# Optimization experiments

Measured on AMD Instinct MI355X. Metric: run time of the kernel, lower is better.

The kernel has to match this reference:

```python
import jax, jax.numpy as jnp
import numpy as np

ATT_RAW = 312
HID = 900
ATT_DIM = 4096


def setup_inputs() -> dict:
    key = jax.random.key(0)
    ks = jax.random.split(key, 12)
    B, S, N, C = 4, 128, 50, ATT_DIM
    x = jax.random.normal(ks[0], (B, S, C), dtype=jnp.float32)
    x_label = jax.random.randint(ks[1], (B, S), 0, N, dtype=jnp.int64)
    att = jax.random.normal(ks[2], (B, N, ATT_RAW), dtype=jnp.float32)
    att_label = jax.random.randint(ks[3], (B, N), 0, N, dtype=jnp.int64)
    def lin(k, out_f, in_f):
        bound = 1.0 / np.sqrt(in_f)
        kw, kb = jax.random.split(k)
        W = jax.random.uniform(kw, (out_f, in_f), jnp.float32, -bound, bound)
        b = jax.random.uniform(kb, (out_f,), jnp.float32, -bound, bound)
        return W, b
    W1, b1 = lin(ks[4], HID, ATT_RAW)       # attnet layer 1
    W2, b2 = lin(ks[5], ATT_DIM, HID)       # attnet layer 2
    W3, b3 = lin(ks[6], HID, 2 * ATT_DIM)   # o layer 1
    W4, b4 = lin(ks[7], 1, HID)             # o layer 2
    return {"x": x, "x_label": x_label, "att": att, "att_label": att_label,
            "W1": W1, "b1": b1, "W2": W2, "b2": b2,
            "W3": W3, "b3": b3, "W4": W4, "b4": b4}


def reference(x, x_label, att, att_label, W1, b1, W2, b2, W3, b3, W4, b4):
    # x: [B,S,C], att: [B,N,312]; train=True branch -> scalar MSE loss
    B, S, C = x.shape
    N = att.shape[1]
    # attnet: 312 -> 900 -> 4096 with ReLU
    att_f = jax.nn.relu(jax.nn.relu(att @ W1.T + b1) @ W2.T + b2)  # [B,N,4096]
    # o layer 1 on concat([x_f, att_f]) == split matmul + broadcast add
    W3x, W3a = W3[:, :C], W3[:, C:]
    hx = jnp.einsum('bsc,hc->bsh', x, W3x)        # [B,S,900]
    ha = jnp.einsum('bnc,hc->bnh', att_f, W3a)    # [B,N,900]
    pre = jax.nn.relu(hx[:, :, None, :] + ha[:, None, :, :] + b3)  # [B,S,N,900]
    score = jax.nn.sigmoid(jnp.einsum('bsnh,h->bsn', pre, W4[0]) + b4[0])  # [B,S,N]
    label = (x_label[:, :, None] == att_label[:, None, :]).astype(score.dtype)
    loss = jnp.sum((label - score) ** 2) / B / S
    return loss
```

## Files before the change

### kernel.cpp

```cpp
#include <hip/hip_runtime.h>
#include <hip/hip_bf16.h>

typedef __attribute__((ext_vector_type(8))) short bf16x8;
typedef __attribute__((ext_vector_type(4))) float f32x4;
typedef __attribute__((ext_vector_type(8))) unsigned short u16x8;

__device__ __forceinline__ void gload16(const void* g, void* l) {
    __builtin_amdgcn_global_load_lds((const __attribute__((address_space(1))) void*)g,
                                     (__attribute__((address_space(3))) void*)l, 16, 0, 0);
}
__device__ __forceinline__ float bf2f(unsigned short u) {
    union { unsigned i; float f; } v; v.i = ((unsigned)u) << 16; return v.f;
}
__device__ __forceinline__ unsigned short f2bf(float f) {
    __hip_bfloat16 h = __float2bfloat16(f);
    return *(unsigned short*)&h;
}

template<int ROWS>
__device__ __forceinline__ void stage_f32(
    const float* __restrict__ src, int ld, int row0, int rmax,
    int k0, int kmax, short* __restrict__ lds, int tid)
{
    #pragma unroll
    for (int i = 0; i < ROWS / 32; ++i) {
        const int ch = i * 256 + tid;
        const int r = ch >> 3;
        const int kc8 = (ch & 7) * 8;
        const int gr = row0 + r;
        const int gk = k0 + kc8;
        u16x8 v;
        if (gr < rmax && gk + 8 <= kmax) {
            const float* s = src + (size_t)gr * ld + gk;
            const float4 f0 = *(const float4*)s;
            const float4 f1 = *(const float4*)(s + 4);
            const float ff[8] = {f0.x, f0.y, f0.z, f0.w, f1.x, f1.y, f1.z, f1.w};
            #pragma unroll
            for (int j = 0; j < 8; ++j) v[j] = f2bf(ff[j]);
        } else if (gr < rmax && gk < kmax) {
            #pragma unroll
            for (int j = 0; j < 8; ++j) {
                float f = 0.f;
                if (gk + j < kmax) f = src[(size_t)gr * ld + gk + j];
                v[j] = f2bf(f);
            }
        } else {
            v = (u16x8){0, 0, 0, 0, 0, 0, 0, 0};
        }
        *(u16x8*)((char*)lds + r * 128 + ((kc8 * 2) ^ ((r & 7) << 4))) = v;
    }
}

template<int ROWS>
__device__ __forceinline__ void stage_gl(const unsigned short* __restrict__ src,
                                         int ld, int row0, int k0,
                                         short* __restrict__ lds, int w, int l)
{
    const int sr0 = w * 8 + (l >> 3);
    const int scb = (l & 7) * 16;
    #pragma unroll
    for (int c = 0; c < ROWS / 32; ++c) {
        const int r = c * 32 + sr0;
        const int cbs = scb ^ ((r & 7) << 4);
        const char* g = (const char*)(src + (size_t)(row0 + r) * ld + k0) + cbs;
        char* dst = (char*)lds + (size_t)(c * 32 + w * 8) * 128;
        gload16(g, dst);
    }
}

struct PadJob {
    const float* src; unsigned short* dst;
    int src_ld, col0, M, K, Kp;
    int chunk_begin;
};
struct PG1Args {
    PadJob j[4]; int total;
    const float *att, *W1, *b1;
    unsigned short* h1;
};

__global__ __launch_bounds__(256)
void padg1(PG1Args P)
{
    __shared__ short As[64 * 64];
    __shared__ short Bs[64 * 64];
    const int gid = blockIdx.x;
    const int tid = threadIdx.x;

    if (gid < 60) {
        const int bm = (gid & 3) * 64, bn = (gid >> 2) * 64;
        const int w = tid >> 6, l = tid & 63;
        const int wm = w >> 1, wn = w & 1;

        f32x4 acc[2][2];
        #pragma unroll
        for (int i = 0; i < 2; ++i)
            #pragma unroll
            for (int j = 0; j < 2; ++j)
                acc[i][j] = (f32x4){0.f, 0.f, 0.f, 0.f};

        for (int k0 = 0; k0 < 320; k0 += 64) {
            stage_f32<64>(P.att, 312, bm, 200, k0, 312, As, tid);
            stage_f32<64>(P.W1,  312, bn, 900, k0, 312, Bs, tid);
            __syncthreads();
            #pragma unroll
            for (int ks = 0; ks < 64; ks += 32) {
                bf16x8 a[2], b[2];
                const int kb = ks * 2 + (l >> 4) * 16;
                #pragma unroll
                for (int i = 0; i < 2; ++i) {
                    const int ra = wm * 32 + i * 16 + (l & 15);
                    a[i] = *(const bf16x8*)((const char*)As + ra * 128 + (kb ^ ((ra & 7) << 4)));
                    const int rb = wn * 32 + i * 16 + (l & 15);
                    b[i] = *(const bf16x8*)((const char*)Bs + rb * 128 + (kb ^ ((rb & 7) << 4)));
                }
                #pragma unroll
                for (int i = 0; i < 2; ++i)
                    #pragma unroll
                    for (int j = 0; j < 2; ++j)
                        acc[i][j] = __builtin_amdgcn_mfma_f32_16x16x32_bf16(a[i], b[j], acc[i][j], 0, 0, 0);
            }
            __syncthreads();
        }

        #pragma unroll
        for (int i = 0; i < 2; ++i) {
            #pragma unroll
            for (int j = 0; j < 2; ++j) {
                const int col = bn + wn * 32 + j * 16 + (l & 15);
                const float bv = (col < 900) ? P.b1[col] : 0.f;
                #pragma unroll
                for (int q = 0; q < 4; ++q) {
                    const int row = bm + wm * 32 + i * 16 + (l >> 4) * 4 + q;
                    float v = fmaxf(acc[i][j][q] + bv, 0.f);
                    if (row >= 200) v = 0.f;
                    P.h1[(size_t)row * 960 + col] = f2bf(v);
                }
            }
        }
        return;
    }

    const int idx = (gid - 60) * 256 + tid;
    if (idx >= P.total) return;
    int ji = 0;
    #pragma unroll
    for (int k = 1; k < 4; ++k) if (idx >= P.j[k].chunk_begin) ji = k;
    const PadJob J = P.j[ji];
    const int cid = idx - J.chunk_begin;
    const int kp8 = J.Kp >> 3;
    const int m = cid / kp8;
    const int kc = (cid - m * kp8) << 3;
    u16x8 v;
    if (m < J.M && kc + 8 <= J.K) {
        const float* s = J.src + (size_t)m * J.src_ld + J.col0 + kc;
        const float4 f0 = *(const float4*)s;
        const float4 f1 = *(const float4*)(s + 4);
        const float ff[8] = {f0.x, f0.y, f0.z, f0.w, f1.x, f1.y, f1.z, f1.w};
        #pragma unroll
        for (int j = 0; j < 8; ++j) v[j] = f2bf(ff[j]);
    } else {
        #pragma unroll
        for (int j = 0; j < 8; ++j) {
            float f = 0.f;
            const int k = kc + j;
            if (m < J.M && k < J.K) f = J.src[(size_t)m * J.src_ld + J.col0 + k];
            v[j] = f2bf(f);
        }
    }
    *(u16x8*)(J.dst + (size_t)m * J.Kp + kc) = v;
}

template<bool RELU, bool BIAS>
__global__ __launch_bounds__(256)
void gemm_mfma64(const unsigned short* __restrict__ A,
                 const unsigned short* __restrict__ B,
                 const float* __restrict__ bias,
                 unsigned short* __restrict__ Cout, int ldc,
                 int Mtrue, int Ntrue, int Kp)
{
    __shared__ short As[64 * 64];
    __shared__ short Bs[64 * 64];
    const int bm = blockIdx.y * 64, bn = blockIdx.x * 64;
    const int tid = threadIdx.x;
    const int w = tid >> 6, l = tid & 63;
    const int wm = w >> 1, wn = w & 1;

    f32x4 acc[2][2];
    #pragma unroll
    for (int i = 0; i < 2; ++i)
        #pragma unroll
        for (int j = 0; j < 2; ++j)
            acc[i][j] = (f32x4){0.f, 0.f, 0.f, 0.f};

    for (int k0 = 0; k0 < Kp; k0 += 64) {
        stage_gl<64>(A, Kp, bm, k0, As, w, l);
        stage_gl<64>(B, Kp, bn, k0, Bs, w, l);
        asm volatile("s_waitcnt vmcnt(0)");
        __syncthreads();

        #pragma unroll
        for (int ks = 0; ks < 64; ks += 32) {
            bf16x8 a[2], b[2];
            const int kb = ks * 2 + (l >> 4) * 16;
            #pragma unroll
            for (int i = 0; i < 2; ++i) {
                const int ra = wm * 32 + i * 16 + (l & 15);
                a[i] = *(const bf16x8*)((const char*)As + ra * 128 + (kb ^ ((ra & 7) << 4)));
                const int rb = wn * 32 + i * 16 + (l & 15);
                b[i] = *(const bf16x8*)((const char*)Bs + rb * 128 + (kb ^ ((rb & 7) << 4)));
            }
            #pragma unroll
            for (int i = 0; i < 2; ++i)
                #pragma unroll
                for (int j = 0; j < 2; ++j)
                    acc[i][j] = __builtin_amdgcn_mfma_f32_16x16x32_bf16(a[i], b[j], acc[i][j], 0, 0, 0);
        }
        __syncthreads();
    }

    #pragma unroll
    for (int i = 0; i < 2; ++i) {
        #pragma unroll
        for (int j = 0; j < 2; ++j) {
            const int col = bn + wn * 32 + j * 16 + (l & 15);
            float bv = 0.f;
            if (BIAS && col < Ntrue) bv = bias[col];
            #pragma unroll
            for (int q = 0; q < 4; ++q) {
                const int row = bm + wm * 32 + i * 16 + (l >> 4) * 4 + q;
                float v = acc[i][j][q] + bv;
                if (RELU) v = fmaxf(v, 0.f);
                if (row >= Mtrue) v = 0.f;
                Cout[(size_t)row * ldc + col] = f2bf(v);
            }
        }
    }
}

struct G34Args {
    const unsigned short *A3, *B3; float* P3;
    const unsigned short *A4, *B4; float* P4;
};

__global__ __launch_bounds__(256)
void gemm128_split(G34Args ga)
{
    __shared__ short As[128 * 64];
    __shared__ short Bs[128 * 64];
    const int tid = threadIdx.x;
    const int w = tid >> 6, l = tid & 63;
    const int wm = w >> 1, wn = w & 1;

    const unsigned short *A, *Bm;
    float* P;
    int by, bx, z, Mtrue;
    const int gid = blockIdx.x;
    if (gid < 256) {
        z = gid >> 5; const int rem = gid & 31; by = rem >> 3; bx = rem & 7;
        A = ga.A3; Bm = ga.B3; P = ga.P3; Mtrue = 512;
    } else {
        const int g2 = gid - 256;
        z = g2 >> 4; const int rem = g2 & 15; by = rem >> 3; bx = rem & 7;
        A = ga.A4; Bm = ga.B4; P = ga.P4; Mtrue = 200;
    }
    const int k_begin = z * 512;

    f32x4 acc[4][4];
    #pragma unroll
    for (int i = 0; i < 4; ++i)
        #pragma unroll
        for (int j = 0; j < 4; ++j)
            acc[i][j] = (f32x4){0.f, 0.f, 0.f, 0.f};

    for (int k0 = k_begin; k0 < k_begin + 512; k0 += 64) {
        stage_gl<128>(A, 4096, by * 128, k0, As, w, l);
        stage_gl<128>(Bm, 4096, bx * 128, k0, Bs, w, l);
        asm volatile("s_waitcnt vmcnt(0)");
        __syncthreads();

        #pragma unroll
        for (int ks = 0; ks < 64; ks += 32) {
            bf16x8 a[4], b[4];
            const int kb = ks * 2 + (l >> 4) * 16;
            #pragma unroll
            for (int i = 0; i < 4; ++i) {
                const int ra = wm * 64 + i * 16 + (l & 15);
                a[i] = *(const bf16x8*)((const char*)As + ra * 128 + (kb ^ ((ra & 7) << 4)));
                const int rb = wn * 64 + i * 16 + (l & 15);
                b[i] = *(const bf16x8*)((const char*)Bs + rb * 128 + (kb ^ ((rb & 7) << 4)));
            }
            #pragma unroll
            for (int i = 0; i < 4; ++i)
                #pragma unroll
                for (int j = 0; j < 4; ++j)
                    acc[i][j] = __builtin_amdgcn_mfma_f32_16x16x32_bf16(a[i], b[j], acc[i][j], 0, 0, 0);
        }
        __syncthreads();
    }

    float* slab = P + (size_t)z * Mtrue * 900;
    #pragma unroll
    for (int i = 0; i < 4; ++i) {
        #pragma unroll
        for (int j = 0; j < 4; ++j) {
            const int col = bx * 128 + wn * 64 + j * 16 + (l & 15);
            if (col >= 900) continue;
            #pragma unroll
            for (int q = 0; q < 4; ++q) {
                const int row = by * 128 + wm * 64 + i * 16 + (l >> 4) * 4 + q;
                if (row < Mtrue)
                    slab[(size_t)row * 900 + col] = acc[i][j][q];
            }
        }
    }
}

__global__ __launch_bounds__(512)
void score_loss(const float* __restrict__ hxp,
                const float* __restrict__ hap,
                const float* __restrict__ b3,
                const float* __restrict__ W4,
                const float* __restrict__ b4,
                const int* __restrict__ xl,
                const int* __restrict__ al,
                float* __restrict__ part)
{
    __shared__ __align__(16) unsigned short hxs[8 * 904];
    __shared__ __align__(16) unsigned short has[16 * 904];
    __shared__ __align__(16) float w4s[904];
    __shared__ float zpart[4][8][16];
    __shared__ float red[2];

    const int tid = threadIdx.x;
    const int nt = blockIdx.x, st = blockIdx.y, b = blockIdx.z;
    const int row0 = b * 128 + st * 8;

    for (int t = tid; t < 24 * 113; t += 512) {
        float f[8] = {0.f, 0.f, 0.f, 0.f, 0.f, 0.f, 0.f, 0.f};
        unsigned short* dst;
        int nv;
        if (t < 8 * 113) {
            const int r = t / 113, c = t - r * 113;
            const int k = c * 8;
            nv = (k + 8 <= 900) ? 8 : 4;
            const int row = row0 + r;
            #pragma unroll 1
            for (int s = 0; s < 8; ++s) {
                const float* p = hxp + ((size_t)s * 512 + row) * 900 + k;
                const float4 a0 = *(const float4*)p;
                f[0] += a0.x; f[1] += a0.y; f[2] += a0.z; f[3] += a0.w;
                if (nv == 8) {
                    const float4 a1 = *(const float4*)(p + 4);
                    f[4] += a1.x; f[5] += a1.y; f[6] += a1.z; f[7] += a1.w;
                }
            }
            const float4 bb0 = *(const float4*)(b3 + k);
            f[0] += bb0.x; f[1] += bb0.y; f[2] += bb0.z; f[3] += bb0.w;
            if (nv == 8) {
                const float4 bb1 = *(const float4*)(b3 + k + 4);
                f[4] += bb1.x; f[5] += bb1.y; f[6] += bb1.z; f[7] += bb1.w;
            }
            dst = hxs + r * 904 + k;
        } else {
            const int t2 = t - 8 * 113;
            const int r = t2 / 113, c = t2 - r * 113;
            const int k = c * 8;
            nv = (k + 8 <= 900) ? 8 : 4;
            const int n = nt * 16 + r;
            if (n < 50) {
                const int row = b * 50 + n;
                #pragma unroll 1
                for (int s = 0; s < 8; ++s) {
                    const float* p = hap + ((size_t)s * 200 + row) * 900 + k;
                    const float4 a0 = *(const float4*)p;
                    f[0] += a0.x; f[1] += a0.y; f[2] += a0.z; f[3] += a0.w;
                    if (nv == 8) {
                        const float4 a1 = *(const float4*)(p + 4);
                        f[4] += a1.x; f[5] += a1.y; f[6] += a1.z; f[7] += a1.w;
                    }
                }
            }
            dst = has + r * 904 + k;
        }
        u16x8 v;
        #pragma unroll
        for (int j = 0; j < 8; ++j) v[j] = f2bf(f[j]);
        if (nv == 4) { v[4] = 0; v[5] = 0; v[6] = 0; v[7] = 0; }
        *(u16x8*)dst = v;
    }
    for (int t = tid; t < 226; t += 512) {
        float4 v = {0.f, 0.f, 0.f, 0.f};
        if (t < 225) v = *(const float4*)(W4 + t * 4);
        *(float4*)(w4s + t * 4) = v;
    }
    __syncthreads();

    const int hs = tid >> 7;
    const int si = (tid >> 4) & 7;
    const int ni = tid & 15;

    float acc = 0.f;
    const unsigned short* hrow = hxs + si * 904;
    const unsigned short* arow = has + ni * 904;
    for (int c = hs; c < 113; c += 4) {
        const u16x8 hv = *(const u16x8*)(hrow + c * 8);
        const u16x8 av = *(const u16x8*)(arow + c * 8);
        const float4 w0 = *(const float4*)(w4s + c * 8);
        const float4 w1 = *(const float4*)(w4s + c * 8 + 4);
        const float ww[8] = {w0.x, w0.y, w0.z, w0.w, w1.x, w1.y, w1.z, w1.w};
        #pragma unroll
        for (int j = 0; j < 8; ++j) {
            const float u = bf2f((unsigned short)hv[j]) + bf2f((unsigned short)av[j]);
            acc = fmaf(fmaxf(u, 0.f), ww[j], acc);
        }
    }
    zpart[hs][si][ni] = acc;
    __syncthreads();

    float dd = 0.f;
    if (tid < 128) {
        const int esi = tid >> 4, eni = tid & 15;
        const int n = nt * 16 + eni;
        const float z = zpart[0][esi][eni] + zpart[1][esi][eni]
                      + zpart[2][esi][eni] + zpart[3][esi][eni] + b4[0];
        const float sc = 1.f / (1.f + __expf(-z));
        if (n < 50) {
            const float lab = (xl[row0 + esi] == al[b * 50 + n]) ? 1.f : 0.f;
            const float d = lab - sc;
            dd = d * d;
        }
        #pragma unroll
        for (int off = 32; off > 0; off >>= 1)
            dd += __shfl_down(dd, off);
        if ((tid & 63) == 0) red[tid >> 6] = dd;
    }
    __syncthreads();
    if (tid == 0)
        part[nt + 4 * (st + 16 * b)] = red[0] + red[1];
}

__global__ __launch_bounds__(256)
void final_loss(const float* __restrict__ part, float* __restrict__ out)
{
    __shared__ float r[4];
    const int tid = threadIdx.x;
    float v = part[tid];
    #pragma unroll
    for (int off = 32; off > 0; off >>= 1)
        v += __shfl_down(v, off);
    if ((tid & 63) == 0) r[tid >> 6] = v;
    __syncthreads();
    if (tid == 0) out[0] = (r[0] + r[1] + r[2] + r[3]) * (1.f / 512.f);
}

extern "C" void kernel_launch(void* const* d_in, const int* in_sizes, int n_in,
                              void* d_out, int out_size, void* d_ws, size_t ws_size,
                              hipStream_t stream)
{
    const float* x   = (const float*)d_in[0];
    const int*   xl  = (const int*)  d_in[1];
    const float* att = (const float*)d_in[2];
    const int*   al  = (const int*)  d_in[3];
    const float* W1  = (const float*)d_in[4];
    const float* b1  = (const float*)d_in[5];
    const float* W2  = (const float*)d_in[6];
    const float* b2  = (const float*)d_in[7];
    const float* W3  = (const float*)d_in[8];
    const float* b3  = (const float*)d_in[9];
    const float* W4  = (const float*)d_in[10];
    const float* b4  = (const float*)d_in[11];
    float* out = (float*)d_out;

    const int B = 4, S = 128, N = 50, C = 4096, H = 900, AR = 312;
    const int MS = B * S;
    const int MN = B * N;
    const int MNp = 256;
    const int Hp = 960;
    const int W3p = 1024;
    const int SPLITS = 8;

    char* base = (char*)d_ws;
    size_t off = 0;
    auto alloc = [&](size_t bytes) { void* r = base + off; off = (off + bytes + 255) & ~(size_t)255; return r; };
    unsigned short* x_bf   = (unsigned short*)alloc((size_t)MS * C * 2);
    unsigned short* W2_bf  = (unsigned short*)alloc((size_t)C * Hp * 2);
    unsigned short* W3x_bf = (unsigned short*)alloc((size_t)W3p * C * 2);
    unsigned short* W3a_bf = (unsigned short*)alloc((size_t)W3p * C * 2);
    unsigned short* h1_bf  = (unsigned short*)alloc((size_t)MNp * Hp * 2);
    unsigned short* attf_bf= (unsigned short*)alloc((size_t)MNp * C * 2);
    float* hxp = (float*)alloc((size_t)SPLITS * MS * H * 4);
    float* hap = (float*)alloc((size_t)SPLITS * MN * H * 4);
    float* part = (float*)alloc(256 * 4);

    const dim3 blk(256);
    auto cdiv = [](int a, int b) { return (a + b - 1) / b; };

    PG1Args P;
    int cb = 0;
    auto setjob = [&](int i, const float* src, unsigned short* dst, int ld, int col0,
                      int M, int K, int Kp, int Mp) {
        P.j[i] = PadJob{src, dst, ld, col0, M, K, Kp, cb};
        cb += Mp * (Kp >> 3);
    };
    setjob(0, x,   x_bf,   C,     0, MS, C,  C,   MS);
    setjob(1, W2,  W2_bf,  H,     0, C,  H,  Hp,  C);
    setjob(2, W3,  W3x_bf, 2 * C, 0, H,  C,  C,   W3p);
    setjob(3, W3,  W3a_bf, 2 * C, C, H,  C,  C,   W3p);
    P.total = cb;
    P.att = att; P.W1 = W1; P.b1 = b1; P.h1 = h1_bf;
    padg1<<<dim3(60 + cdiv(cb, 256)), blk, 0, stream>>>(P);

    gemm_mfma64<true, true><<<dim3(C / 64, MNp / 64), blk, 0, stream>>>(
        h1_bf, W2_bf, b2, attf_bf, C, MN, C, Hp);

    G34Args ga{x_bf, W3x_bf, hxp, attf_bf, W3a_bf, hap};
    gemm128_split<<<dim3(384), blk, 0, stream>>>(ga);

    score_loss<<<dim3(4, 16, 4), dim3(512), 0, stream>>>(hxp, hap, b3, W4, b4, xl, al, part);
    final_loss<<<dim3(1), blk, 0, stream>>>(part, out);
}
```

Before: 82.63 us.

## Co-schedule independent GEMMs in shared launches and precompute bf16 split-K reductions

The x·W3x GEMM does not depend on the attnet path, so it now runs in the same launch as the W2 GEMM. The att·W3a GEMM runs alongside the hx split-K reduction. Split-K goes from 8 to 16, which gives more blocks per launch but doubles the partial-sum traffic. The split-K reduction moves out of score_loss into separate passes that write bf16 hx/ha once, instead of each score block re-reducing the fp32 partials redundantly. This adds one extra kernel launch and more workspace.

```diff
diff --git a/kernel.cpp b/kernel.cpp
--- a/kernel.cpp
+++ b/kernel.cpp
@@ -66,6 +66,151 @@
         char* dst = (char*)lds + (size_t)(c * 32 + w * 8) * 128;
         gload16(g, dst);
     }
+}
+
+__device__ __forceinline__ void gemm64_body(
+    const unsigned short* __restrict__ A, const unsigned short* __restrict__ B,
+    const float* __restrict__ bias, unsigned short* __restrict__ Cout, int ldc,
+    int bm, int bn, int Kp, int Mtrue,
+    short* As, short* Bs, int tid)
+{
+    const int w = tid >> 6, l = tid & 63;
+    const int wm = w >> 1, wn = w & 1;
+    f32x4 acc[2][2];
+    #pragma unroll
+    for (int i = 0; i < 2; ++i)
+        #pragma unroll
+        for (int j = 0; j < 2; ++j)
+            acc[i][j] = (f32x4){0.f, 0.f, 0.f, 0.f};
+
+    for (int k0 = 0; k0 < Kp; k0 += 64) {
+        stage_gl<64>(A, Kp, bm, k0, As, w, l);
+        stage_gl<64>(B, Kp, bn, k0, Bs, w, l);
+        asm volatile("s_waitcnt vmcnt(0)");
+        __syncthreads();
+        #pragma unroll
+        for (int ks = 0; ks < 64; ks += 32) {
+            bf16x8 a[2], b[2];
+            const int kb = ks * 2 + (l >> 4) * 16;
+            #pragma unroll
+            for (int i = 0; i < 2; ++i) {
+                const int ra = wm * 32 + i * 16 + (l & 15);
+                a[i] = *(const bf16x8*)((const char*)As + ra * 128 + (kb ^ ((ra & 7) << 4)));
+                const int rb = wn * 32 + i * 16 + (l & 15);
+                b[i] = *(const bf16x8*)((const char*)Bs + rb * 128 + (kb ^ ((rb & 7) << 4)));
+            }
+            #pragma unroll
+            for (int i = 0; i < 2; ++i)
+                #pragma unroll
+                for (int j = 0; j < 2; ++j)
+                    acc[i][j] = __builtin_amdgcn_mfma_f32_16x16x32_bf16(a[i], b[j], acc[i][j], 0, 0, 0);
+        }
+        __syncthreads();
+    }
+
+    #pragma unroll
+    for (int i = 0; i < 2; ++i) {
+        #pragma unroll
+        for (int j = 0; j < 2; ++j) {
+            const int col = bn + wn * 32 + j * 16 + (l & 15);
+            const float bv = bias[col];
+            #pragma unroll
+            for (int q = 0; q < 4; ++q) {
+                const int row = bm + wm * 32 + i * 16 + (l >> 4) * 4 + q;
+                float v = fmaxf(acc[i][j][q] + bv, 0.f);
+                if (row >= Mtrue) v = 0.f;
+                Cout[(size_t)row * ldc + col] = f2bf(v);
+            }
+        }
+    }
+}
+
+__device__ __forceinline__ void gemm128_body(
+    const unsigned short* __restrict__ A, const unsigned short* __restrict__ B,
+    float* __restrict__ slab, int by, int bx, int k_begin, int k_steps, int Mtrue,
+    short* As, short* Bs, int tid)
+{
+    const int w = tid >> 6, l = tid & 63;
+    const int wm = w >> 1, wn = w & 1;
+    f32x4 acc[4][4];
+    #pragma unroll
+    for (int i = 0; i < 4; ++i)
+        #pragma unroll
+        for (int j = 0; j < 4; ++j)
+            acc[i][j] = (f32x4){0.f, 0.f, 0.f, 0.f};
+
+    for (int t = 0; t < k_steps; ++t) {
+        const int k0 = k_begin + t * 64;
+        stage_gl<128>(A, 4096, by * 128, k0, As, w, l);
+        stage_gl<128>(B, 4096, bx * 128, k0, Bs, w, l);
+        asm volatile("s_waitcnt vmcnt(0)");
+        __syncthreads();
+        #pragma unroll
+        for (int ks = 0; ks < 64; ks += 32) {
+            bf16x8 a[4], b[4];
+            const int kb = ks * 2 + (l >> 4) * 16;
+            #pragma unroll
+            for (int i = 0; i < 4; ++i) {
+                const int ra = wm * 64 + i * 16 + (l & 15);
+                a[i] = *(const bf16x8*)((const char*)As + ra * 128 + (kb ^ ((ra & 7) << 4)));
+                const int rb = wn * 64 + i * 16 + (l & 15);
+                b[i] = *(const bf16x8*)((const char*)Bs + rb * 128 + (kb ^ ((rb & 7) << 4)));
+            }
+            #pragma unroll
+            for (int i = 0; i < 4; ++i)
+                #pragma unroll
+                for (int j = 0; j < 4; ++j)
+                    acc[i][j] = __builtin_amdgcn_mfma_f32_16x16x32_bf16(a[i], b[j], acc[i][j], 0, 0, 0);
+        }
+        __syncthreads();
+    }
+
+    #pragma unroll
+    for (int i = 0; i < 4; ++i) {
+        #pragma unroll
+        for (int j = 0; j < 4; ++j) {
+            const int col = bx * 128 + wn * 64 + j * 16 + (l & 15);
+            if (col >= 900) continue;
+            #pragma unroll
+            for (int q = 0; q < 4; ++q) {
+                const int row = by * 128 + wm * 64 + i * 16 + (l >> 4) * 4 + q;
+                if (row < Mtrue)
+                    slab[(size_t)row * 900 + col] = acc[i][j][q];
+            }
+        }
+    }
+}
+
+__device__ __forceinline__ void reduce16(const float* __restrict__ p,
+                                         const float* __restrict__ bias,
+                                         unsigned short* __restrict__ o,
+                                         int M, int idx)
+{
+    const int m = idx / 113;
+    const int c = idx - m * 113;
+    const int k = c * 8;
+    u16x8 v;
+    #pragma unroll
+    for (int q = 0; q < 8; q += 4) {
+        if (k + q < 900) {
+            float4 a = *(const float4*)(p + (size_t)m * 900 + k + q);
+            #pragma unroll 1
+            for (int s = 1; s < 16; ++s) {
+                const float4 t = *(const float4*)(p + ((size_t)s * M + m) * 900 + k + q);
+                a.x += t.x; a.y += t.y; a.z += t.z; a.w += t.w;
+            }
+            if (bias) {
+                const float4 bb = *(const float4*)(bias + k + q);
+                a.x += bb.x; a.y += bb.y; a.z += bb.z; a.w += bb.w;
+            }
+            v[q + 0] = f2bf(a.x); v[q + 1] = f2bf(a.y);
+            v[q + 2] = f2bf(a.z); v[q + 3] = f2bf(a.w);
+        } else {
+            #pragma unroll
+            for (int j = 0; j < 4; ++j) v[q + j] = 0;
+        }
+    }
+    *(u16x8*)(o + (size_t)m * 904 + k) = v;
 }
 
 struct PadJob {
@@ -171,155 +316,64 @@
     *(u16x8*)(J.dst + (size_t)m * J.Kp + kc) = v;
 }
 
-template<bool RELU, bool BIAS>
+struct G23Args {
+    const unsigned short *h1, *W2; const float* b2; unsigned short* attf;
+    const unsigned short *xb, *W3x; float* hxp;
+};
+
 __global__ __launch_bounds__(256)
-void gemm_mfma64(const unsigned short* __restrict__ A,
-                 const unsigned short* __restrict__ B,
-                 const float* __restrict__ bias,
-                 unsigned short* __restrict__ Cout, int ldc,
-                 int Mtrue, int Ntrue, int Kp)
-{
-    __shared__ short As[64 * 64];
-    __shared__ short Bs[64 * 64];
-    const int bm = blockIdx.y * 64, bn = blockIdx.x * 64;
-    const int tid = threadIdx.x;
-    const int w = tid >> 6, l = tid & 63;
-    const int wm = w >> 1, wn = w & 1;
-
-    f32x4 acc[2][2];
-    #pragma unroll
-    for (int i = 0; i < 2; ++i)
-        #pragma unroll
-        for (int j = 0; j < 2; ++j)
-            acc[i][j] = (f32x4){0.f, 0.f, 0.f, 0.f};
-
-    for (int k0 = 0; k0 < Kp; k0 += 64) {
-        stage_gl<64>(A, Kp, bm, k0, As, w, l);
-        stage_gl<64>(B, Kp, bn, k0, Bs, w, l);
-        asm volatile("s_waitcnt vmcnt(0)");
-        __syncthreads();
-
-        #pragma unroll
-        for (int ks = 0; ks < 64; ks += 32) {
-            bf16x8 a[2], b[2];
-            const int kb = ks * 2 + (l >> 4) * 16;
-            #pragma unroll
-            for (int i = 0; i < 2; ++i) {
-                const int ra = wm * 32 + i * 16 + (l & 15);
-                a[i] = *(const bf16x8*)((const char*)As + ra * 128 + (kb ^ ((ra & 7) << 4)));
-                const int rb = wn * 32 + i * 16 + (l & 15);
-                b[i] = *(const bf16x8*)((const char*)Bs + rb * 128 + (kb ^ ((rb & 7) << 4)));
-            }
-            #pragma unroll
-            for (int i = 0; i < 2; ++i)
-                #pragma unroll
-                for (int j = 0; j < 2; ++j)
-                    acc[i][j] = __builtin_amdgcn_mfma_f32_16x16x32_bf16(a[i], b[j], acc[i][j], 0, 0, 0);
-        }
-        __syncthreads();
-    }
-
-    #pragma unroll
-    for (int i = 0; i < 2; ++i) {
-        #pragma unroll
-        for (int j = 0; j < 2; ++j) {
-            const int col = bn + wn * 32 + j * 16 + (l & 15);
-            float bv = 0.f;
-            if (BIAS && col < Ntrue) bv = bias[col];
-            #pragma unroll
-            for (int q = 0; q < 4; ++q) {
-                const int row = bm + wm * 32 + i * 16 + (l >> 4) * 4 + q;
-                float v = acc[i][j][q] + bv;
-                if (RELU) v = fmaxf(v, 0.f);
-                if (row >= Mtrue) v = 0.f;
-                Cout[(size_t)row * ldc + col] = f2bf(v);
-            }
-        }
-    }
-}
-
-struct G34Args {
-    const unsigned short *A3, *B3; float* P3;
-    const unsigned short *A4, *B4; float* P4;
-};
-
-__global__ __launch_bounds__(256)
-void gemm128_split(G34Args ga)
+void g2g3(G23Args a)
 {
     __shared__ short As[128 * 64];
     __shared__ short Bs[128 * 64];
+    const int gid = blockIdx.x;
     const int tid = threadIdx.x;
-    const int w = tid >> 6, l = tid & 63;
-    const int wm = w >> 1, wn = w & 1;
-
-    const unsigned short *A, *Bm;
-    float* P;
-    int by, bx, z, Mtrue;
+
+    if (gid < 256) {
+        const int bm = (gid >> 6) * 64, bn = (gid & 63) * 64;
+        gemm64_body(a.h1, a.W2, a.b2, a.attf, 4096, bm, bn, 960, 200, As, Bs, tid);
+    } else {
+        const int g3 = gid - 256;
+        const int z = g3 >> 5, by = (g3 >> 3) & 3, bx = g3 & 7;
+        gemm128_body(a.xb, a.W3x, a.hxp + (size_t)z * 512 * 900,
+                     by, bx, z * 256, 4, 512, As, Bs, tid);
+    }
+}
+
+struct G4RArgs {
+    const unsigned short *attf, *W3a; float* hap;
+    const float *hxp, *b3; unsigned short* hx_bf;
+};
+
+__global__ __launch_bounds__(256)
+void g4redhx(G4RArgs a)
+{
+    __shared__ short As[128 * 64];
+    __shared__ short Bs[128 * 64];
     const int gid = blockIdx.x;
+    const int tid = threadIdx.x;
+
     if (gid < 256) {
-        z = gid >> 5; const int rem = gid & 31; by = rem >> 3; bx = rem & 7;
-        A = ga.A3; Bm = ga.B3; P = ga.P3; Mtrue = 512;
+        const int z = gid >> 4, by = (gid >> 3) & 1, bx = gid & 7;
+        gemm128_body(a.attf, a.W3a, a.hap + (size_t)z * 200 * 900,
+                     by, bx, z * 256, 4, 200, As, Bs, tid);
     } else {
-        const int g2 = gid - 256;
-        z = g2 >> 4; const int rem = g2 & 15; by = rem >> 3; bx = rem & 7;
-        A = ga.A4; Bm = ga.B4; P = ga.P4; Mtrue = 200;
-    }
-    const int k_begin = z * 512;
-
-    f32x4 acc[4][4];
-    #pragma unroll
-    for (int i = 0; i < 4; ++i)
-        #pragma unroll
-        for (int j = 0; j < 4; ++j)
-            acc[i][j] = (f32x4){0.f, 0.f, 0.f, 0.f};
-
-    for (int k0 = k_begin; k0 < k_begin + 512; k0 += 64) {
-        stage_gl<128>(A, 4096, by * 128, k0, As, w, l);
-        stage_gl<128>(Bm, 4096, bx * 128, k0, Bs, w, l);
-        asm volatile("s_waitcnt vmcnt(0)");
-        __syncthreads();
-
-        #pragma unroll
-        for (int ks = 0; ks < 64; ks += 32) {
-            bf16x8 a[4], b[4];
-            const int kb = ks * 2 + (l >> 4) * 16;
-            #pragma unroll
-            for (int i = 0; i < 4; ++i) {
-                const int ra = wm * 64 + i * 16 + (l & 15);
-                a[i] = *(const bf16x8*)((const char*)As + ra * 128 + (kb ^ ((ra & 7) << 4)));
-                const int rb = wn * 64 + i * 16 + (l & 15);
-                b[i] = *(const bf16x8*)((const char*)Bs + rb * 128 + (kb ^ ((rb & 7) << 4)));
-            }
-            #pragma unroll
-            for (int i = 0; i < 4; ++i)
-                #pragma unroll
-                for (int j = 0; j < 4; ++j)
-                    acc[i][j] = __builtin_amdgcn_mfma_f32_16x16x32_bf16(a[i], b[j], acc[i][j], 0, 0, 0);
-        }
-        __syncthreads();
-    }
-
-    float* slab = P + (size_t)z * Mtrue * 900;
-    #pragma unroll
-    for (int i = 0; i < 4; ++i) {
-        #pragma unroll
-        for (int j = 0; j < 4; ++j) {
-            const int col = bx * 128 + wn * 64 + j * 16 + (l & 15);
-            if (col >= 900) continue;
-            #pragma unroll
-            for (int q = 0; q < 4; ++q) {
-                const int row = by * 128 + wm * 64 + i * 16 + (l >> 4) * 4 + q;
-                if (row < Mtrue)
-                    slab[(size_t)row * 900 + col] = acc[i][j][q];
-            }
-        }
-    }
+        const int idx = (gid - 256) * 256 + tid;
+        reduce16(a.hxp, a.b3, a.hx_bf, 512, idx);
+    }
+}
+
+__global__ __launch_bounds__(256)
+void reduce_ha(const float* __restrict__ hap, unsigned short* __restrict__ ha_bf)
+{
+    const int idx = blockIdx.x * 256 + threadIdx.x;
+    if (idx >= 200 * 113) return;
+    reduce16(hap, nullptr, ha_bf, 200, idx);
 }
 
 __global__ __launch_bounds__(512)
-void score_loss(const float* __restrict__ hxp,
-                const float* __restrict__ hap,
-                const float* __restrict__ b3,
+void score_loss(const unsigned short* __restrict__ hxb,
+                const unsigned short* __restrict__ hab,
                 const float* __restrict__ W4,
                 const float* __restrict__ b4,
                 const int* __restrict__ xl,
@@ -337,56 +391,20 @@
     const int row0 = b * 128 + st * 8;
 
     for (int t = tid; t < 24 * 113; t += 512) {
-        float f[8] = {0.f, 0.f, 0.f, 0.f, 0.f, 0.f, 0.f, 0.f};
+        u16x8 v;
         unsigned short* dst;
-        int nv;
         if (t < 8 * 113) {
             const int r = t / 113, c = t - r * 113;
-            const int k = c * 8;
-            nv = (k + 8 <= 900) ? 8 : 4;
-            const int row = row0 + r;
-            #pragma unroll 1
-            for (int s = 0; s < 8; ++s) {
-                const float* p = hxp + ((size_t)s * 512 + row) * 900 + k;
-                const float4 a0 = *(const float4*)p;
-                f[0] += a0.x; f[1] += a0.y; f[2] += a0.z; f[3] += a0.w;
-                if (nv == 8) {
-                    const float4 a1 = *(const float4*)(p + 4);
-                    f[4] += a1.x; f[5] += a1.y; f[6] += a1.z; f[7] += a1.w;
-                }
-            }
-            const float4 bb0 = *(const float4*)(b3 + k);
-            f[0] += bb0.x; f[1] += bb0.y; f[2] += bb0.z; f[3] += bb0.w;
-            if (nv == 8) {
-                const float4 bb1 = *(const float4*)(b3 + k + 4);
-                f[4] += bb1.x; f[5] += bb1.y; f[6] += bb1.z; f[7] += bb1.w;
-            }
-            dst = hxs + r * 904 + k;
+            v = *(const u16x8*)(hxb + (size_t)(row0 + r) * 904 + c * 8);
+            dst = hxs + r * 904 + c * 8;
         } else {
             const int t2 = t - 8 * 113;
             const int r = t2 / 113, c = t2 - r * 113;
-            const int k = c * 8;
-            nv = (k + 8 <= 900) ? 8 : 4;
             const int n = nt * 16 + r;
-            if (n < 50) {
-                const int row = b * 50 + n;
-                #pragma unroll 1
-                for (int s = 0; s < 8; ++s) {
-                    const float* p = hap + ((size_t)s * 200 + row) * 900 + k;
-                    const float4 a0 = *(const float4*)p;
-                    f[0] += a0.x; f[1] += a0.y; f[2] += a0.z; f[3] += a0.w;
-                    if (nv == 8) {
-                        const float4 a1 = *(const float4*)(p + 4);
-                        f[4] += a1.x; f[5] += a1.y; f[6] += a1.z; f[7] += a1.w;
-                    }
-                }
-            }
-            dst = has + r * 904 + k;
-        }
-        u16x8 v;
-        #pragma unroll
-        for (int j = 0; j < 8; ++j) v[j] = f2bf(f[j]);
-        if (nv == 4) { v[4] = 0; v[5] = 0; v[6] = 0; v[7] = 0; }
+            if (n < 50) v = *(const u16x8*)(hab + (size_t)(b * 50 + n) * 904 + c * 8);
+            else        v = (u16x8){0,0,0,0,0,0,0,0};
+            dst = has + r * 904 + c * 8;
+        }
         *(u16x8*)dst = v;
     }
     for (int t = tid; t < 226; t += 512) {
@@ -478,7 +496,7 @@
     const int MNp = 256;
     const int Hp = 960;
     const int W3p = 1024;
-    const int SPLITS = 8;
+    const int SPL = 16;
 
     char* base = (char*)d_ws;
     size_t off = 0;
@@ -489,8 +507,10 @@
     unsigned short* W3a_bf = (unsigned short*)alloc((size_t)W3p * C * 2);
     unsigned short* h1_bf  = (unsigned short*)alloc((size_t)MNp * Hp * 2);
     unsigned short* attf_bf= (unsigned short*)alloc((size_t)MNp * C * 2);
-    float* hxp = (float*)alloc((size_t)SPLITS * MS * H * 4);
-    float* hap = (float*)alloc((size_t)SPLITS * MN * H * 4);
+    float* hxp = (float*)alloc((size_t)SPL * MS * H * 4);
+    float* hap = (float*)alloc((size_t)SPL * MN * H * 4);
+    unsigned short* hx_bf = (unsigned short*)alloc((size_t)MS * 904 * 2);
+    unsigned short* ha_bf = (unsigned short*)alloc((size_t)MN * 904 * 2);
     float* part = (float*)alloc(256 * 4);
 
     const dim3 blk(256);
@@ -511,12 +531,14 @@
     P.att = att; P.W1 = W1; P.b1 = b1; P.h1 = h1_bf;
     padg1<<<dim3(60 + cdiv(cb, 256)), blk, 0, stream>>>(P);
 
-    gemm_mfma64<true, true><<<dim3(C / 64, MNp / 64), blk, 0, stream>>>(
-        h1_bf, W2_bf, b2, attf_bf, C, MN, C, Hp);
-
-    G34Args ga{x_bf, W3x_bf, hxp, attf_bf, W3a_bf, hap};
-    gemm128_split<<<dim3(384), blk, 0, stream>>>(ga);
-
-    score_loss<<<dim3(4, 16, 4), dim3(512), 0, stream>>>(hxp, hap, b3, W4, b4, xl, al, part);
+    G23Args a23{h1_bf, W2_bf, b2, attf_bf, x_bf, W3x_bf, hxp};
+    g2g3<<<dim3(768), blk, 0, stream>>>(a23);
+
+    G4RArgs a4r{attf_bf, W3a_bf, hap, hxp, b3, hx_bf};
+    g4redhx<<<dim3(482), blk, 0, stream>>>(a4r);
+
+    reduce_ha<<<dim3(cdiv(MN * 113, 256)), blk, 0, stream>>>(hap, ha_bf);
+
+    score_loss<<<dim3(4, 16, 4), dim3(512), 0, stream>>>(hx_bf, ha_bf, W4, b4, xl, al, part);
     final_loss<<<dim3(1), blk, 0, stream>>>(part, out);
 }
```

Measured after the change: 75.10 us. 1.1x faster.

## Hoist split-K reduction into a separate kernel and fuse final loss via atomics

Applied to the files above, without the earlier changes.

Moves the reduction of split-K partial sums for hx and ha out of score_loss into a dedicated kernel that writes bf16 padded rows once. This removes the repeated re-reading of the fp32 partial slabs by every score block. The final reduction kernel is replaced by an atomicAdd into the output, which is zeroed in the first kernel. This adds one launch and an extra bf16 round trip through memory, and makes the summation order nondeterministic.

```diff
diff --git a/kernel.cpp b/kernel.cpp
--- a/kernel.cpp
+++ b/kernel.cpp
@@ -77,6 +77,7 @@
     PadJob j[4]; int total;
     const float *att, *W1, *b1;
     unsigned short* h1;
+    float* out;
 };
 
 __global__ __launch_bounds__(256)
@@ -141,6 +142,8 @@
         return;
     }
 
+    if (gid == 60 && tid == 0) P.out[0] = 0.f;
+
     const int idx = (gid - 60) * 256 + tid;
     if (idx >= P.total) return;
     int ji = 0;
@@ -316,15 +319,55 @@
     }
 }
 
+__global__ __launch_bounds__(256)
+void reduce_both(const float* __restrict__ hxp, const float* __restrict__ hap,
+                 const float* __restrict__ b3,
+                 unsigned short* __restrict__ hx_bf, unsigned short* __restrict__ ha_bf)
+{
+    int idx = blockIdx.x * 256 + threadIdx.x;
+    const int HX = 512 * 113;
+    const float* p; unsigned short* o; const float* bias; int M;
+    if (idx < HX) { p = hxp; o = hx_bf; bias = b3; M = 512; }
+    else {
+        idx -= HX;
+        if (idx >= 200 * 113) return;
+        p = hap; o = ha_bf; bias = nullptr; M = 200;
+    }
+    const int m = idx / 113;
+    const int c = idx - m * 113;
+    const int k = c * 8;
+    u16x8 v;
+    #pragma unroll
+    for (int q = 0; q < 8; q += 4) {
+        if (k + q < 900) {
+            float4 a = *(const float4*)(p + (size_t)m * 900 + k + q);
+            #pragma unroll 1
+            for (int s = 1; s < 8; ++s) {
+                const float4 t = *(const float4*)(p + ((size_t)s * M + m) * 900 + k + q);
+                a.x += t.x; a.y += t.y; a.z += t.z; a.w += t.w;
+            }
+            if (bias) {
+                const float4 bb = *(const float4*)(bias + k + q);
+                a.x += bb.x; a.y += bb.y; a.z += bb.z; a.w += bb.w;
+            }
+            v[q + 0] = f2bf(a.x); v[q + 1] = f2bf(a.y);
+            v[q + 2] = f2bf(a.z); v[q + 3] = f2bf(a.w);
+        } else {
+            #pragma unroll
+            for (int j = 0; j < 4; ++j) v[q + j] = 0;
+        }
+    }
+    *(u16x8*)(o + (size_t)m * 904 + k) = v;
+}
+
 __global__ __launch_bounds__(512)
-void score_loss(const float* __restrict__ hxp,
-                const float* __restrict__ hap,
-                const float* __restrict__ b3,
+void score_loss(const unsigned short* __restrict__ hxb,
+                const unsigned short* __restrict__ hab,
                 const float* __restrict__ W4,
                 const float* __restrict__ b4,
                 const int* __restrict__ xl,
                 const int* __restrict__ al,
-                float* __restrict__ part)
+                float* __restrict__ out)
 {
     __shared__ __align__(16) unsigned short hxs[8 * 904];
     __shared__ __align__(16) unsigned short has[16 * 904];
@@ -337,56 +380,20 @@
     const int row0 = b * 128 + st * 8;
 
     for (int t = tid; t < 24 * 113; t += 512) {
-        float f[8] = {0.f, 0.f, 0.f, 0.f, 0.f, 0.f, 0.f, 0.f};
+        u16x8 v;
         unsigned short* dst;
-        int nv;
         if (t < 8 * 113) {
             const int r = t / 113, c = t - r * 113;
-            const int k = c * 8;
-            nv = (k + 8 <= 900) ? 8 : 4;
-            const int row = row0 + r;
-            #pragma unroll 1
-            for (int s = 0; s < 8; ++s) {
-                const float* p = hxp + ((size_t)s * 512 + row) * 900 + k;
-                const float4 a0 = *(const float4*)p;
-                f[0] += a0.x; f[1] += a0.y; f[2] += a0.z; f[3] += a0.w;
-                if (nv == 8) {
-                    const float4 a1 = *(const float4*)(p + 4);
-                    f[4] += a1.x; f[5] += a1.y; f[6] += a1.z; f[7] += a1.w;
-                }
-            }
-            const float4 bb0 = *(const float4*)(b3 + k);
-            f[0] += bb0.x; f[1] += bb0.y; f[2] += bb0.z; f[3] += bb0.w;
-            if (nv == 8) {
-                const float4 bb1 = *(const float4*)(b3 + k + 4);
-                f[4] += bb1.x; f[5] += bb1.y; f[6] += bb1.z; f[7] += bb1.w;
-            }
-            dst = hxs + r * 904 + k;
+            v = *(const u16x8*)(hxb + (size_t)(row0 + r) * 904 + c * 8);
+            dst = hxs + r * 904 + c * 8;
         } else {
             const int t2 = t - 8 * 113;
             const int r = t2 / 113, c = t2 - r * 113;
-            const int k = c * 8;
-            nv = (k + 8 <= 900) ? 8 : 4;
             const int n = nt * 16 + r;
-            if (n < 50) {
-                const int row = b * 50 + n;
-                #pragma unroll 1
-                for (int s = 0; s < 8; ++s) {
-                    const float* p = hap + ((size_t)s * 200 + row) * 900 + k;
-                    const float4 a0 = *(const float4*)p;
-                    f[0] += a0.x; f[1] += a0.y; f[2] += a0.z; f[3] += a0.w;
-                    if (nv == 8) {
-                        const float4 a1 = *(const float4*)(p + 4);
-                        f[4] += a1.x; f[5] += a1.y; f[6] += a1.z; f[7] += a1.w;
-                    }
-                }
-            }
-            dst = has + r * 904 + k;
-        }
-        u16x8 v;
-        #pragma unroll
-        for (int j = 0; j < 8; ++j) v[j] = f2bf(f[j]);
-        if (nv == 4) { v[4] = 0; v[5] = 0; v[6] = 0; v[7] = 0; }
+            if (n < 50) v = *(const u16x8*)(hab + (size_t)(b * 50 + n) * 904 + c * 8);
+            else        v = (u16x8){0,0,0,0,0,0,0,0};
+            dst = has + r * 904 + c * 8;
+        }
         *(u16x8*)dst = v;
     }
     for (int t = tid; t < 226; t += 512) {
@@ -437,21 +444,7 @@
     }
     __syncthreads();
     if (tid == 0)
-        part[nt + 4 * (st + 16 * b)] = red[0] + red[1];
-}
-
-__global__ __launch_bounds__(256)
-void final_loss(const float* __restrict__ part, float* __restrict__ out)
-{
-    __shared__ float r[4];
-    const int tid = threadIdx.x;
-    float v = part[tid];
-    #pragma unroll
-    for (int off = 32; off > 0; off >>= 1)
-        v += __shfl_down(v, off);
-    if ((tid & 63) == 0) r[tid >> 6] = v;
-    __syncthreads();
-    if (tid == 0) out[0] = (r[0] + r[1] + r[2] + r[3]) * (1.f / 512.f);
+        atomicAdd(out, (red[0] + red[1]) * (1.f / 512.f));
 }
 
 extern "C" void kernel_launch(void* const* d_in, const int* in_sizes, int n_in,
@@ -491,7 +484,8 @@
     unsigned short* attf_bf= (unsigned short*)alloc((size_t)MNp * C * 2);
     float* hxp = (float*)alloc((size_t)SPLITS * MS * H * 4);
     float* hap = (float*)alloc((size_t)SPLITS * MN * H * 4);
-    float* part = (float*)alloc(256 * 4);
+    unsigned short* hx_bf = (unsigned short*)alloc((size_t)MS * 904 * 2);
+    unsigned short* ha_bf = (unsigned short*)alloc((size_t)MN * 904 * 2);
 
     const dim3 blk(256);
     auto cdiv = [](int a, int b) { return (a + b - 1) / b; };
@@ -508,7 +502,7 @@
     setjob(2, W3,  W3x_bf, 2 * C, 0, H,  C,  C,   W3p);
     setjob(3, W3,  W3a_bf, 2 * C, C, H,  C,  C,   W3p);
     P.total = cb;
-    P.att = att; P.W1 = W1; P.b1 = b1; P.h1 = h1_bf;
+    P.att = att; P.W1 = W1; P.b1 = b1; P.h1 = h1_bf; P.out = out;
     padg1<<<dim3(60 + cdiv(cb, 256)), blk, 0, stream>>>(P);
 
     gemm_mfma64<true, true><<<dim3(C / 64, MNp / 64), blk, 0, stream>>>(
@@ -517,6 +511,7 @@
     G34Args ga{x_bf, W3x_bf, hxp, attf_bf, W3a_bf, hap};
     gemm128_split<<<dim3(384), blk, 0, stream>>>(ga);
 
-    score_loss<<<dim3(4, 16, 4), dim3(512), 0, stream>>>(hxp, hap, b3, W4, b4, xl, al, part);
-    final_loss<<<dim3(1), blk, 0, stream>>>(part, out);
-}
+    reduce_both<<<cdiv((MS + MN) * 113, 256), blk, 0, stream>>>(hxp, hap, b3, hx_bf, ha_bf);
+
+    score_loss<<<dim3(4, 16, 4), dim3(512), 0, stream>>>(hx_bf, ha_bf, W4, b4, xl, al, out);
+}
```

Result: faster. 69.15 us, median of 2 (-16.3%).
